# Performance work log

Hardware: AMD Instinct MI355X
Metric: run time of the kernel (lower is better)

The kernel has to match this reference:

```python
import jax, jax.numpy as jnp
import numpy as np

D, A, H, FF = 1024, 128, 8, 4096
B, S = 4, 2048
EPS = 1e-5


def setup_inputs() -> dict:
    key = jax.random.key(0)
    ks = jax.random.split(key, 12)
    s = 0.02
    return {
        "x": jax.random.normal(ks[0], (B, S, D), dtype=jnp.float32),
        # per-head QKV projections, stacked over heads: [H, D, A]
        "Wq": jax.random.normal(ks[1], (H, D, A), dtype=jnp.float32) * s,
        "bq": jnp.zeros((H, A), dtype=jnp.float32),
        "Wk": jax.random.normal(ks[2], (H, D, A), dtype=jnp.float32) * s,
        "bk": jnp.zeros((H, A), dtype=jnp.float32),
        "Wv": jax.random.normal(ks[3], (H, D, A), dtype=jnp.float32) * s,
        "bv": jnp.zeros((H, A), dtype=jnp.float32),
        "Wo": jax.random.normal(ks[4], (A, D), dtype=jnp.float32) * s,
        "bo": jnp.zeros((D,), dtype=jnp.float32),
        "g1": jnp.ones((D,), dtype=jnp.float32),
        "beta1": jnp.zeros((D,), dtype=jnp.float32),
        "g2": jnp.ones((D,), dtype=jnp.float32),
        "beta2": jnp.zeros((D,), dtype=jnp.float32),
        "W1": jax.random.normal(ks[5], (D, FF), dtype=jnp.float32) * s,
        "bf1": jnp.zeros((FF,), dtype=jnp.float32),
        "W2": jax.random.normal(ks[6], (FF, D), dtype=jnp.float32) * s,
        "bf2": jnp.zeros((D,), dtype=jnp.float32),
    }


def _layernorm(x, g, b):
    mu = jnp.mean(x, axis=-1, keepdims=True)
    var = jnp.mean(jnp.square(x - mu), axis=-1, keepdims=True)
    return (x - mu) * jax.lax.rsqrt(var + EPS) * g + b


def reference(x, Wq, bq, Wk, bk, Wv, bv, Wo, bo, g1, beta1, g2, beta2, W1, bf1, W2, bf2):
    scale = jnp.sqrt(jnp.float32(A))
    # per-head projections, batched over heads: [H, B, S, A]
    q = jnp.einsum("bsd,hda->hbsa", x, Wq) + bq[:, None, None, :]
    k = jnp.einsum("bsd,hda->hbsa", x, Wk) + bk[:, None, None, :]
    v = jnp.einsum("bsd,hda->hbsa", x, Wv) + bv[:, None, None, :]
    scores = jnp.einsum("hbqa,hbka->hbqk", q, k) / scale  # [H,B,S,S]
    attn = jax.nn.softmax(scores, axis=-1)
    # heads are SUMMED (not concatenated): sum over h -> [B,S,A]
    head_sum = jnp.einsum("hbqk,hbka->bqa", attn, v)
    attn_out = head_sum @ Wo + bo  # [B,S,D]
    x = _layernorm(x + attn_out, g1, beta1)
    h = jax.nn.relu(x @ W1 + bf1)
    ff = h @ W2 + bf2
    return _layernorm(x + ff, g2, beta2)
```

## Files before the change

### kernel.cpp

```cpp
#include <hip/hip_runtime.h>
#include <hip/hip_bf16.h>
#include <stdint.h>

#define DD 1024
#define AA 128
#define HH 8
#define FF 4096
#define BB 4
#define SS 2048
#define MM (BB*SS)
#define EPSV 1e-5f

typedef __bf16 bf16x8 __attribute__((ext_vector_type(8)));
typedef __bf16 bf16x4 __attribute__((ext_vector_type(4)));
typedef float  f32x4  __attribute__((ext_vector_type(4)));
typedef float  f32x16 __attribute__((ext_vector_type(16)));

__device__ __forceinline__ void gload_lds16(const void* g, void* l) {
  __builtin_amdgcn_global_load_lds(
      (const __attribute__((address_space(1))) uint32_t*)(uintptr_t)g,
      (__attribute__((address_space(3))) uint32_t*)(uintptr_t)l, 16, 0, 0);
}

__global__ __launch_bounds__(256) void transpose_conv(const float* __restrict__ in,
                                                      __bf16* __restrict__ out,
                                                      int rows, int cols) {
  __shared__ float tile[64][65];
  const int r0 = blockIdx.y * 64, c0 = blockIdx.x * 64;
  for (int i = threadIdx.x; i < 4096; i += 256) {
    int r = i >> 6, c = i & 63;
    tile[r][c] = in[(long)(r0 + r) * cols + c0 + c];
  }
  __syncthreads();
  for (int i = threadIdx.x; i < 4096; i += 256) {
    int c = i >> 6, r = i & 63;
    out[(long)(c0 + c) * rows + r0 + r] = (__bf16)tile[r][c];
  }
}

__global__ __launch_bounds__(256) void transpose_qkv(const float* __restrict__ Wq,
                                                     const float* __restrict__ Wk,
                                                     const float* __restrict__ Wv,
                                                     __bf16* __restrict__ out) {
  __shared__ float tile[64][65];
  const int z = blockIdx.z;
  const int p = z >> 3, h = z & 7;
  const float* in = ((p == 0) ? Wq : (p == 1) ? Wk : Wv) + (long)h * DD * AA;
  __bf16* o = out + (long)(p * 1024 + h * 128) * DD;
  const int r0 = blockIdx.y * 64, c0 = blockIdx.x * 64;
  for (int i = threadIdx.x; i < 4096; i += 256) {
    int r = i >> 6, c = i & 63;
    tile[r][c] = in[(long)(r0 + r) * AA + c0 + c];
  }
  __syncthreads();
  for (int i = threadIdx.x; i < 4096; i += 256) {
    int c = i >> 6, r = i & 63;
    o[(long)(c0 + c) * DD + r0 + r] = (__bf16)tile[r][c];
  }
}

__global__ void build_qkv_bias(const float* __restrict__ bq, const float* __restrict__ bk,
                               const float* __restrict__ bv, float* __restrict__ out) {
  int i = blockIdx.x * 256 + threadIdx.x;
  if (i < 3072) {
    const float* src = (i < 1024) ? bq : (i < 2048) ? bk : bv;
    out[i] = src[i & 1023];
  }
}

__global__ void conv_f32_bf16(const float* __restrict__ in, __bf16* __restrict__ out, int n4) {
  int i = blockIdx.x * 256 + threadIdx.x;
  if (i < n4) {
    float4 v = ((const float4*)in)[i];
    bf16x4 o = { (__bf16)v.x, (__bf16)v.y, (__bf16)v.z, (__bf16)v.w };
    ((bf16x4*)out)[i] = o;
  }
}

template<bool RELU, bool RESID, bool OUTF, bool OUTB, bool WRVT>
__global__ __launch_bounds__(256) void gemm_bt(
    const __bf16* __restrict__ Ag, const __bf16* __restrict__ Bt,
    const float* __restrict__ bias, const float* __restrict__ resid,
    float* __restrict__ Cf, __bf16* __restrict__ Cb, __bf16* __restrict__ vTb,
    int M, int N, int K)
{
  __shared__ __bf16 As[128 * 32];
  __shared__ __bf16 Bs[128 * 32];
  const int t = threadIdx.x;
  const int w = t >> 6, l = t & 63;
  const int gx = gridDim.x, nwg = gx * gridDim.y;
  int bid = blockIdx.y * gx + blockIdx.x;
  int swz = (bid & 7) * (nwg >> 3) + (bid >> 3);
  const int m0 = (swz / gx) * 128, n0 = (swz % gx) * 128;
  const int wr = w >> 1, wc = w & 1;
  const int lr = l & 15, lg = l >> 4;

  f32x4 acc[4][4] = {};

  const __bf16* gA = Ag + (long)(m0 + w * 32 + (l >> 2)) * K + (l & 3) * 8;
  const __bf16* gB = Bt + (long)(n0 + w * 32 + (l >> 2)) * K + (l & 3) * 8;
  __bf16* lA = &As[w * 1024];
  __bf16* lB = &Bs[w * 1024];

  for (int k0 = 0; k0 < K; k0 += 32) {
    gload_lds16(gA + k0, lA);
    gload_lds16(gA + (long)16 * K + k0, lA + 512);
    gload_lds16(gB + k0, lB);
    gload_lds16(gB + (long)16 * K + k0, lB + 512);
    __syncthreads();
    bf16x8 af[4], bfr[4];
#pragma unroll
    for (int mi = 0; mi < 4; mi++)
      af[mi] = *(const bf16x8*)&As[(wr * 64 + mi * 16 + lr) * 32 + lg * 8];
#pragma unroll
    for (int nj = 0; nj < 4; nj++)
      bfr[nj] = *(const bf16x8*)&Bs[(wc * 64 + nj * 16 + lr) * 32 + lg * 8];
#pragma unroll
    for (int mi = 0; mi < 4; mi++)
#pragma unroll
      for (int nj = 0; nj < 4; nj++)
        acc[mi][nj] = __builtin_amdgcn_mfma_f32_16x16x32_bf16(af[mi], bfr[nj], acc[mi][nj], 0, 0, 0);
    __syncthreads();
  }

#pragma unroll
  for (int mi = 0; mi < 4; mi++) {
    const int row0 = m0 + wr * 64 + mi * 16 + lg * 4;
#pragma unroll
    for (int nj = 0; nj < 4; nj++) {
      const int col = n0 + wc * 64 + nj * 16 + lr;
      const float bv = bias[col];
#pragma unroll
      for (int rg = 0; rg < 4; rg++) {
        const int row = row0 + rg;
        float v = acc[mi][nj][rg] + bv;
        if constexpr (RESID) v += resid[(long)row * N + col];
        if constexpr (RELU)  v = fmaxf(v, 0.f);
        if constexpr (OUTF)  Cf[(long)row * N + col] = v;
        if constexpr (OUTB)  Cb[(long)row * N + col] = (__bf16)v;
        if constexpr (WRVT) {
          if (col >= 2048) {
            int h = (col - 2048) >> 7, a = col & 127;
            int b = row >> 11, s = row & 2047;
            vTb[(((long)(b * 8 + h)) * 128 + a) * 2048 + s] = (__bf16)v;
          }
        }
      }
    }
  }
}

__global__ __launch_bounds__(256) void attn_kernel(
    const __bf16* __restrict__ qkv,
    const __bf16* __restrict__ vT,
    float* __restrict__ hsp)
{
  __shared__ __bf16 Ks[64 * 128];
  __shared__ __bf16 Vs[128 * 64];
  const int t = threadIdx.x, w = t >> 6, l = t & 63;
  const int q32 = l & 31, hi = l >> 5;
  const int h = blockIdx.y, b = blockIdx.z;
  const long rowbase = (long)b * SS + blockIdx.x * 128 + w * 32;
  const float C2 = (float)(0.08838834764831845 * 1.44269504088896340);

  bf16x8 qf[8];
  {
    const __bf16* qrow = qkv + (rowbase + q32) * 3072 + h * 128;
#pragma unroll
    for (int ks = 0; ks < 8; ks++) qf[ks] = *(const bf16x8*)(qrow + ks * 16 + hi * 8);
  }

  float mrun = -1e30f, lrun = 0.f;
  f32x16 O[4] = {};

  const __bf16* kbase = qkv + (long)b * SS * 3072 + 1024 + h * 128;
  const __bf16* vbase = vT + ((long)(b * 8 + h) * 128) * 2048;

  for (int kt = 0; kt < 32; kt++) {
    const int kv0 = kt * 64;
#pragma unroll
    for (int i = 0; i < 4; i++) {
      const int cb = (i * 4 + w) * 64;
      const int rK = (cb + l) >> 4, cK = l & 15;
      gload_lds16(kbase + (long)(kv0 + rK) * 3072 + ((cK ^ (rK & 15)) << 3),
                  (char*)Ks + cb * 16);
      const int aV = (cb >> 3) + (l >> 3), cV = l & 7;
      gload_lds16(vbase + (long)aV * 2048 + kv0 + ((cV ^ (aV & 7)) << 3),
                  (char*)Vs + cb * 16);
    }
    __syncthreads();

    f32x16 st[2] = {};
#pragma unroll
    for (int s2 = 0; s2 < 2; s2++) {
      const int r = s2 * 32 + q32;
#pragma unroll
      for (int ks = 0; ks < 8; ks++) {
        const int g = (2 * ks + hi) ^ (r & 15);
        bf16x8 kf = *(const bf16x8*)((const char*)Ks + r * 256 + (g << 4));
        st[s2] = __builtin_amdgcn_mfma_f32_32x32x16_bf16(kf, qf[ks], st[s2], 0, 0, 0);
      }
    }

    float pmax = st[0][0];
#pragma unroll
    for (int s2 = 0; s2 < 2; s2++)
#pragma unroll
      for (int rg = 0; rg < 16; rg++) pmax = fmaxf(pmax, st[s2][rg]);
    pmax = fmaxf(pmax, __shfl_xor(pmax, 32));

    if (!__all(pmax - mrun <= 64.f)) {
      const float mnew = fmaxf(mrun, pmax);
      const float sscl = exp2f((mrun - mnew) * C2);
      lrun *= sscl;
      mrun = mnew;
      float ssb[16];
#pragma unroll
      for (int rg = 0; rg < 16; rg++)
        ssb[rg] = __shfl(sscl, (l & 32) + ((rg & 3) + 8 * (rg >> 2) + 4 * hi));
#pragma unroll
      for (int aj = 0; aj < 4; aj++)
#pragma unroll
        for (int rg = 0; rg < 16; rg++) O[aj][rg] *= ssb[rg];
    }

    float rsum = 0.f;
#pragma unroll
    for (int s2 = 0; s2 < 2; s2++)
#pragma unroll
      for (int rg = 0; rg < 16; rg++) {
        const float p = exp2f((st[s2][rg] - mrun) * C2);
        st[s2][rg] = p;
        rsum += p;
      }
    rsum += __shfl_xor(rsum, 32);
    lrun += rsum;

#pragma unroll
    for (int c = 0; c < 4; c++) {
      const int sA = (2 * c) >> 2, tA = (2 * c) & 3;
      const int sB = (2 * c + 1) >> 2, tB = (2 * c + 1) & 3;
      uint32_t W01a, W23a, W01b, W23b;
      asm("v_cvt_pk_bf16_f32 %0, %1, %2" : "=v"(W01a) : "v"(st[sA][4*tA+0]), "v"(st[sA][4*tA+1]));
      asm("v_cvt_pk_bf16_f32 %0, %1, %2" : "=v"(W23a) : "v"(st[sA][4*tA+2]), "v"(st[sA][4*tA+3]));
      asm("v_cvt_pk_bf16_f32 %0, %1, %2" : "=v"(W01b) : "v"(st[sB][4*tB+0]), "v"(st[sB][4*tB+1]));
      asm("v_cvt_pk_bf16_f32 %0, %1, %2" : "=v"(W23b) : "v"(st[sB][4*tB+2]), "v"(st[sB][4*tB+3]));
      const uint32_t X01 = __shfl_xor(hi ? W01a : W01b, 32);
      const uint32_t X23 = __shfl_xor(hi ? W23a : W23b, 32);
      union { uint32_t u[4]; bf16x8 v; } pa;
      pa.u[0] = hi ? X01 : W01a;
      pa.u[1] = hi ? X23 : W23a;
      pa.u[2] = hi ? W01b : X01;
      pa.u[3] = hi ? W23b : X23;
#pragma unroll
      for (int aj = 0; aj < 4; aj++) {
        const int a = aj * 32 + q32;
        const int gv = (2 * c + hi) ^ (a & 7);
        bf16x8 vf = *(const bf16x8*)((const char*)Vs + a * 128 + (gv << 4));
        O[aj] = __builtin_amdgcn_mfma_f32_32x32x16_bf16(pa.v, vf, O[aj], 0, 0, 0);
      }
    }
    __syncthreads();
  }

  const float invl = 1.f / lrun;
  float invb[16];
#pragma unroll
  for (int rg = 0; rg < 16; rg++)
    invb[rg] = __shfl(invl, (l & 32) + ((rg & 3) + 8 * (rg >> 2) + 4 * hi));
  float* ho = hsp + ((long)h * MM + rowbase) * AA;
#pragma unroll
  for (int aj = 0; aj < 4; aj++)
#pragma unroll
    for (int rg = 0; rg < 16; rg++) {
      const int qr = (rg & 3) + 8 * (rg >> 2) + 4 * hi;
      ho[(long)qr * AA + aj * 32 + q32] = O[aj][rg] * invb[rg];
    }
}

__global__ __launch_bounds__(256) void reduce_heads(const float* __restrict__ hsp,
                                                    __bf16* __restrict__ out) {
  const long i = (long)blockIdx.x * 256 + threadIdx.x;
  const float4* p = (const float4*)hsp;
  float4 s = p[i];
#pragma unroll
  for (int h = 1; h < 8; h++) {
    float4 v = p[i + (long)h * (MM * AA / 4)];
    s.x += v.x; s.y += v.y; s.z += v.z; s.w += v.w;
  }
  bf16x4 o = { (__bf16)s.x, (__bf16)s.y, (__bf16)s.z, (__bf16)s.w };
  ((bf16x4*)out)[i] = o;
}

template<bool WB>
__global__ __launch_bounds__(256) void ln_kernel(
    const float* __restrict__ in, const float* __restrict__ g, const float* __restrict__ be,
    float* __restrict__ outf, __bf16* __restrict__ outb)
{
  const int row = blockIdx.x, t = threadIdx.x;
  const float4 xv = *(const float4*)(in + (long)row * DD + t * 4);
  float s = xv.x + xv.y + xv.z + xv.w;
  float s2 = xv.x * xv.x + xv.y * xv.y + xv.z * xv.z + xv.w * xv.w;
#pragma unroll
  for (int off = 32; off >= 1; off >>= 1) {
    s += __shfl_down(s, off);
    s2 += __shfl_down(s2, off);
  }
  __shared__ float sm[4], sm2[4];
  __shared__ float mu_s, rs_s;
  const int wid = t >> 6;
  if ((t & 63) == 0) { sm[wid] = s; sm2[wid] = s2; }
  __syncthreads();
  if (t == 0) {
    float S = sm[0] + sm[1] + sm[2] + sm[3];
    float S2 = sm2[0] + sm2[1] + sm2[2] + sm2[3];
    float mu = S * (1.f / 1024.f);
    float var = S2 * (1.f / 1024.f) - mu * mu;
    mu_s = mu;
    rs_s = rsqrtf(var + EPSV);
  }
  __syncthreads();
  const float mu = mu_s, rs = rs_s;
  const float4 gv = *(const float4*)(g + t * 4);
  const float4 bv = *(const float4*)(be + t * 4);
  float o0 = (xv.x - mu) * rs * gv.x + bv.x;
  float o1 = (xv.y - mu) * rs * gv.y + bv.y;
  float o2 = (xv.z - mu) * rs * gv.z + bv.z;
  float o3 = (xv.w - mu) * rs * gv.w + bv.w;
  float4 ov = { o0, o1, o2, o3 };
  *(float4*)(outf + (long)row * DD + t * 4) = ov;
  if constexpr (WB) {
    bf16x4 ob = { (__bf16)o0, (__bf16)o1, (__bf16)o2, (__bf16)o3 };
    *(bf16x4*)(outb + (long)row * DD + t * 4) = ob;
  }
}

extern "C" void kernel_launch(void* const* d_in, const int* in_sizes, int n_in,
                              void* d_out, int out_size, void* d_ws, size_t ws_size,
                              hipStream_t stream) {
  const float* x    = (const float*)d_in[0];
  const float* Wq   = (const float*)d_in[1];
  const float* bq   = (const float*)d_in[2];
  const float* Wk   = (const float*)d_in[3];
  const float* bk   = (const float*)d_in[4];
  const float* Wv   = (const float*)d_in[5];
  const float* bv   = (const float*)d_in[6];
  const float* Wo   = (const float*)d_in[7];
  const float* bo   = (const float*)d_in[8];
  const float* g1   = (const float*)d_in[9];
  const float* be1  = (const float*)d_in[10];
  const float* g2   = (const float*)d_in[11];
  const float* be2  = (const float*)d_in[12];
  const float* W1   = (const float*)d_in[13];
  const float* bf1  = (const float*)d_in[14];
  const float* W2   = (const float*)d_in[15];
  const float* bf2  = (const float*)d_in[16];

  const size_t MB = 1ull << 20;
  char* ws = (char*)d_ws;
  __bf16* WqkvT    = (__bf16*)(ws + 0);
  float*  qkv_bias = (float*) (ws + 6 * MB);
  __bf16* WoT      = (__bf16*)(ws + 7 * MB);
  __bf16* W1T      = (__bf16*)(ws + 8 * MB);
  __bf16* W2T      = (__bf16*)(ws + 16 * MB);
  __bf16* xb       = (__bf16*)(ws + 24 * MB);
  __bf16* qkvb     = (__bf16*)(ws + 40 * MB);
  __bf16* vTb      = (__bf16*)(ws + 88 * MB);
  float*  hsp      = (float*) (ws + 104 * MB);
  __bf16* hs_b     = (__bf16*)(ws + 136 * MB);
  float*  tt       = (float*) (ws + 104 * MB);
  float*  yy       = (float*) (ws + 140 * MB);
  __bf16* yb       = (__bf16*)(ws + 172 * MB);
  __bf16* hb       = (__bf16*)(ws + 24 * MB);

  transpose_qkv<<<dim3(2, 16, 24), 256, 0, stream>>>(Wq, Wk, Wv, WqkvT);
  build_qkv_bias<<<12, 256, 0, stream>>>(bq, bk, bv, qkv_bias);
  transpose_conv<<<dim3(16, 2), 256, 0, stream>>>(Wo, WoT, 128, 1024);
  transpose_conv<<<dim3(64, 16), 256, 0, stream>>>(W1, W1T, 1024, 4096);
  transpose_conv<<<dim3(16, 64), 256, 0, stream>>>(W2, W2T, 4096, 1024);
  conv_f32_bf16<<<8192, 256, 0, stream>>>(x, xb, MM * DD / 4);

  gemm_bt<false, false, false, true, true><<<dim3(24, 64), 256, 0, stream>>>(
      xb, WqkvT, qkv_bias, nullptr, nullptr, qkvb, vTb, MM, 3072, 1024);

  attn_kernel<<<dim3(16, 8, 4), 256, 0, stream>>>(qkvb, vTb, hsp);
  reduce_heads<<<MM * AA / 4 / 256, 256, 0, stream>>>(hsp, hs_b);

  gemm_bt<false, true, true, false, false><<<dim3(8, 64), 256, 0, stream>>>(
      hs_b, WoT, bo, x, tt, nullptr, nullptr, MM, 1024, 128);
  ln_kernel<true><<<MM, 256, 0, stream>>>(tt, g1, be1, yy, yb);

  gemm_bt<true, false, false, true, false><<<dim3(32, 64), 256, 0, stream>>>(
      yb, W1T, bf1, nullptr, nullptr, hb, nullptr, MM, FF, 1024);
  gemm_bt<false, true, true, false, false><<<dim3(8, 64), 256, 0, stream>>>(
      hb, W2T, bf2, yy, tt, nullptr, nullptr, MM, DD, FF);
  ln_kernel<false><<<MM, 256, 0, stream>>>(tt, g2, be2, (float*)d_out, nullptr);
}
```

Measured before the change: 653.6 us.

## Double-buffer attention K/V tiles and move V transpose to a separate kernel

The attention kernel now double-buffers its K and V LDS tiles. The next tile's global-to-LDS loads are issued before the current tile's MFMA work, and the MFMA sections are wrapped in s_setprio. The scattered transposed-V store is removed from the QKV GEMM epilogue and replaced by a dedicated tiled transpose kernel that reads the V slice of the QKV buffer. Together these aim to hide load latency in attention and remove uncoalesced 2-byte strided writes from the GEMM, at the cost of twice the LDS per block (possibly lower occupancy) and an extra kernel launch with its own read and write pass over V.

```diff
diff --git a/kernel.cpp b/kernel.cpp
--- a/kernel.cpp
+++ b/kernel.cpp
@@ -59,6 +59,24 @@
   }
 }
 
+__global__ __launch_bounds__(256) void transpose_v(const __bf16* __restrict__ qkvb,
+                                                   __bf16* __restrict__ vTb) {
+  __shared__ float tile[64][65];
+  const int s0 = blockIdx.x * 64, a0 = blockIdx.y * 64;
+  const int bh = blockIdx.z, b = bh >> 3, h = bh & 7;
+  const __bf16* src = qkvb + ((long)b * SS) * 3072 + 2048 + h * 128;
+  for (int i = threadIdx.x; i < 4096; i += 256) {
+    int r = i >> 6, c = i & 63;
+    tile[r][c] = (float)src[(long)(s0 + r) * 3072 + a0 + c];
+  }
+  __syncthreads();
+  __bf16* dst = vTb + ((long)bh * 128) * 2048;
+  for (int i = threadIdx.x; i < 4096; i += 256) {
+    int c = i >> 6, r = i & 63;
+    dst[(long)(a0 + c) * 2048 + s0 + r] = (__bf16)tile[r][c];
+  }
+}
+
 __global__ void build_qkv_bias(const float* __restrict__ bq, const float* __restrict__ bk,
                                const float* __restrict__ bv, float* __restrict__ out) {
   int i = blockIdx.x * 256 + threadIdx.x;
@@ -77,11 +95,11 @@
   }
 }
 
-template<bool RELU, bool RESID, bool OUTF, bool OUTB, bool WRVT>
+template<bool RELU, bool RESID, bool OUTF, bool OUTB>
 __global__ __launch_bounds__(256) void gemm_bt(
     const __bf16* __restrict__ Ag, const __bf16* __restrict__ Bt,
     const float* __restrict__ bias, const float* __restrict__ resid,
-    float* __restrict__ Cf, __bf16* __restrict__ Cb, __bf16* __restrict__ vTb,
+    float* __restrict__ Cf, __bf16* __restrict__ Cb,
     int M, int N, int K)
 {
   __shared__ __bf16 As[128 * 32];
@@ -138,13 +156,6 @@
         if constexpr (RELU)  v = fmaxf(v, 0.f);
         if constexpr (OUTF)  Cf[(long)row * N + col] = v;
         if constexpr (OUTB)  Cb[(long)row * N + col] = (__bf16)v;
-        if constexpr (WRVT) {
-          if (col >= 2048) {
-            int h = (col - 2048) >> 7, a = col & 127;
-            int b = row >> 11, s = row & 2047;
-            vTb[(((long)(b * 8 + h)) * 128 + a) * 2048 + s] = (__bf16)v;
-          }
-        }
       }
     }
   }
@@ -155,14 +166,17 @@
     const __bf16* __restrict__ vT,
     float* __restrict__ hsp)
 {
-  __shared__ __bf16 Ks[64 * 128];
-  __shared__ __bf16 Vs[128 * 64];
+  __shared__ __bf16 Ks[2][64 * 128];
+  __shared__ __bf16 Vs[2][128 * 64];
   const int t = threadIdx.x, w = t >> 6, l = t & 63;
   const int q32 = l & 31, hi = l >> 5;
   const int h = blockIdx.y, b = blockIdx.z;
   const long rowbase = (long)b * SS + blockIdx.x * 128 + w * 32;
   const float C2 = (float)(0.08838834764831845 * 1.44269504088896340);
 
+  const __bf16* kbase = qkv + (long)b * SS * 3072 + 1024 + h * 128;
+  const __bf16* vbase = vT + ((long)(b * 8 + h) * 128) * 2048;
+
   bf16x8 qf[8];
   {
     const __bf16* qrow = qkv + (rowbase + q32) * 3072 + h * 128;
@@ -173,34 +187,40 @@
   float mrun = -1e30f, lrun = 0.f;
   f32x16 O[4] = {};
 
-  const __bf16* kbase = qkv + (long)b * SS * 3072 + 1024 + h * 128;
-  const __bf16* vbase = vT + ((long)(b * 8 + h) * 128) * 2048;
+#define STAGE(BUF, KV0)                                                              \
+  {                                                                                  \
+    _Pragma("unroll")                                                                \
+    for (int i = 0; i < 4; i++) {                                                    \
+      const int cb = (i * 4 + w) * 64;                                               \
+      const int rK = (cb + l) >> 4, cK = l & 15;                                     \
+      gload_lds16(kbase + (long)((KV0) + rK) * 3072 + ((cK ^ (rK & 15)) << 3),       \
+                  (char*)Ks[BUF] + cb * 16);                                         \
+      const int aV = (cb >> 3) + (l >> 3), cV = l & 7;                               \
+      gload_lds16(vbase + (long)aV * 2048 + (KV0) + ((cV ^ (aV & 7)) << 3),          \
+                  (char*)Vs[BUF] + cb * 16);                                         \
+    }                                                                                \
+  }
+
+  STAGE(0, 0);
+  __syncthreads();
+  int cur = 0;
 
   for (int kt = 0; kt < 32; kt++) {
-    const int kv0 = kt * 64;
-#pragma unroll
-    for (int i = 0; i < 4; i++) {
-      const int cb = (i * 4 + w) * 64;
-      const int rK = (cb + l) >> 4, cK = l & 15;
-      gload_lds16(kbase + (long)(kv0 + rK) * 3072 + ((cK ^ (rK & 15)) << 3),
-                  (char*)Ks + cb * 16);
-      const int aV = (cb >> 3) + (l >> 3), cV = l & 7;
-      gload_lds16(vbase + (long)aV * 2048 + kv0 + ((cV ^ (aV & 7)) << 3),
-                  (char*)Vs + cb * 16);
-    }
-    __syncthreads();
+    if (kt < 31) STAGE(cur ^ 1, (kt + 1) * 64);
 
     f32x16 st[2] = {};
+    __builtin_amdgcn_s_setprio(1);
 #pragma unroll
     for (int s2 = 0; s2 < 2; s2++) {
       const int r = s2 * 32 + q32;
 #pragma unroll
       for (int ks = 0; ks < 8; ks++) {
         const int g = (2 * ks + hi) ^ (r & 15);
-        bf16x8 kf = *(const bf16x8*)((const char*)Ks + r * 256 + (g << 4));
+        bf16x8 kf = *(const bf16x8*)((const char*)Ks[cur] + r * 256 + (g << 4));
         st[s2] = __builtin_amdgcn_mfma_f32_32x32x16_bf16(kf, qf[ks], st[s2], 0, 0, 0);
       }
     }
+    __builtin_amdgcn_s_setprio(0);
 
     float pmax = st[0][0];
 #pragma unroll
@@ -236,6 +256,7 @@
     rsum += __shfl_xor(rsum, 32);
     lrun += rsum;
 
+    __builtin_amdgcn_s_setprio(1);
 #pragma unroll
     for (int c = 0; c < 4; c++) {
       const int sA = (2 * c) >> 2, tA = (2 * c) & 3;
@@ -256,12 +277,16 @@
       for (int aj = 0; aj < 4; aj++) {
         const int a = aj * 32 + q32;
         const int gv = (2 * c + hi) ^ (a & 7);
-        bf16x8 vf = *(const bf16x8*)((const char*)Vs + a * 128 + (gv << 4));
+        bf16x8 vf = *(const bf16x8*)((const char*)Vs[cur] + a * 128 + (gv << 4));
         O[aj] = __builtin_amdgcn_mfma_f32_32x32x16_bf16(pa.v, vf, O[aj], 0, 0, 0);
       }
     }
+    __builtin_amdgcn_s_setprio(0);
+
     __syncthreads();
-  }
+    cur ^= 1;
+  }
+#undef STAGE
 
   const float invl = 1.f / lrun;
   float invb[16];
@@ -380,19 +405,20 @@
   transpose_conv<<<dim3(16, 64), 256, 0, stream>>>(W2, W2T, 4096, 1024);
   conv_f32_bf16<<<8192, 256, 0, stream>>>(x, xb, MM * DD / 4);
 
-  gemm_bt<false, false, false, true, true><<<dim3(24, 64), 256, 0, stream>>>(
-      xb, WqkvT, qkv_bias, nullptr, nullptr, qkvb, vTb, MM, 3072, 1024);
+  gemm_bt<false, false, false, true><<<dim3(24, 64), 256, 0, stream>>>(
+      xb, WqkvT, qkv_bias, nullptr, nullptr, qkvb, MM, 3072, 1024);
+  transpose_v<<<dim3(32, 2, 32), 256, 0, stream>>>(qkvb, vTb);
 
   attn_kernel<<<dim3(16, 8, 4), 256, 0, stream>>>(qkvb, vTb, hsp);
   reduce_heads<<<MM * AA / 4 / 256, 256, 0, stream>>>(hsp, hs_b);
 
-  gemm_bt<false, true, true, false, false><<<dim3(8, 64), 256, 0, stream>>>(
-      hs_b, WoT, bo, x, tt, nullptr, nullptr, MM, 1024, 128);
+  gemm_bt<false, true, true, false><<<dim3(8, 64), 256, 0, stream>>>(
+      hs_b, WoT, bo, x, tt, nullptr, MM, 1024, 128);
   ln_kernel<true><<<MM, 256, 0, stream>>>(tt, g1, be1, yy, yb);
 
-  gemm_bt<true, false, false, true, false><<<dim3(32, 64), 256, 0, stream>>>(
-      yb, W1T, bf1, nullptr, nullptr, hb, nullptr, MM, FF, 1024);
-  gemm_bt<false, true, true, false, false><<<dim3(8, 64), 256, 0, stream>>>(
-      hb, W2T, bf2, yy, tt, nullptr, nullptr, MM, DD, FF);
+  gemm_bt<true, false, false, true><<<dim3(32, 64), 256, 0, stream>>>(
+      yb, W1T, bf1, nullptr, nullptr, hb, MM, FF, 1024);
+  gemm_bt<false, true, true, false><<<dim3(8, 64), 256, 0, stream>>>(
+      hb, W2T, bf2, yy, tt, nullptr, MM, DD, FF);
   ln_kernel<false><<<MM, 256, 0, stream>>>(tt, g2, be2, (float*)d_out, nullptr);
 }
```

Result: faster. 610.0 us (-6.7%).
